# Kernel tuning notes

Measured on AMD Instinct MI355X. Metric: run time of the kernel, lower is better.

Reference implementation:

```python
import jax, jax.numpy as jnp
import numpy as np

B, T, D = 32, 1024, 192
HIDDEN = 4
CH = D * HIDDEN          # conv hidden channels = in_channel * hidden_size
K1, K2 = 5, 3
PAD = 3                  # (K1 - 1) // 2 + 1 for odd kernel_size=5 (ReplicationPad1d)
NUM_LEVELS = 3
N_NODES = 2 ** NUM_LEVELS - 1  # 7 Interaction blocks in the SCINet tree
OUT_LEN = 512


def setup_inputs() -> dict:
    key = jax.random.key(0)
    ks = jax.random.split(key, 6)
    s1 = 1.0 / np.sqrt(D * K1)   # torch Conv1d default init bound (fan_in = Cin*k)
    s2 = 1.0 / np.sqrt(CH * K2)
    sp = 1.0 / np.sqrt(T)
    x = jax.random.normal(ks[0], (B, T, D), dtype=jnp.float32)
    # Stacked params for all 7 tree nodes x 4 branches (phi, psi, eta, rho)
    W1 = jax.random.uniform(ks[1], (N_NODES, 4, CH, D, K1), jnp.float32, -s1, s1)
    b1 = jax.random.uniform(ks[2], (N_NODES, 4, CH), jnp.float32, -s1, s1)
    W2 = jax.random.uniform(ks[3], (N_NODES, 4, D, CH, K2), jnp.float32, -s2, s2)
    b2 = jax.random.uniform(ks[4], (N_NODES, 4, D), jnp.float32, -s2, s2)
    # projection1 = Conv1d(input_len, output_len, k=1, bias=False) over time-as-channels
    Wproj = jax.random.uniform(ks[5], (OUT_LEN, T), jnp.float32, -sp, sp)
    return {"x": x, "W1": W1, "b1": b1, "W2": W2, "b2": b2, "Wproj": Wproj}


def _conv1d(x, w, b):
    # x: (B, Cin, L), w: (Cout, Cin, K)
    y = jax.lax.conv_general_dilated(x, w, (1,), 'VALID',
                                     dimension_numbers=('NCH', 'OIH', 'NCH'))
    return y + b[None, :, None]


def _branch(x, w1, b1, w2, b2):
    # ReplicationPad1d(3,3) -> Conv(k=5) -> LeakyReLU -> (Dropout p=0) -> Conv(k=3) -> Tanh
    xp = jnp.pad(x, ((0, 0), (0, 0), (PAD, PAD)), mode='edge')
    h = jax.nn.leaky_relu(_conv1d(xp, w1, b1), 0.01)
    return jnp.tanh(_conv1d(h, w2, b2))  # length back to L


def _interact(x, w1, b1, w2, b2):
    # x: (B, T, D) -> even/odd (B, D, T/2)
    xe = jnp.transpose(x[:, ::2, :], (0, 2, 1))
    xo = jnp.transpose(x[:, 1::2, :], (0, 2, 1))
    d = xo * jnp.exp(_branch(xe, w1[0], b1[0], w2[0], b2[0]))  # phi
    c = xe * jnp.exp(_branch(xo, w1[1], b1[1], w2[1], b2[1]))  # psi
    even_up = c + _branch(d, w1[2], b1[2], w2[2], b2[2])        # eta
    odd_up = d - _branch(c, w1[3], b1[3], w2[3], b2[3])         # rho
    return jnp.transpose(even_up, (0, 2, 1)), jnp.transpose(odd_up, (0, 2, 1))


def _zip_up(even, odd):
    # interleave even/odd along time (equal lengths since T % 2**levels == 0)
    b, t, c = even.shape
    return jnp.stack([even, odd], axis=2).reshape(b, 2 * t, c)


def _tree(x, level, idx, W1, b1, W2, b2):
    i = idx[0]
    idx[0] += 1
    e, o = _interact(x, W1[i], b1[i], W2[i], b2[i])
    if level == 0:
        return _zip_up(e, o)
    return _zip_up(_tree(e, level - 1, idx, W1, b1, W2, b2),
                   _tree(o, level - 1, idx, W1, b1, W2, b2))


def reference(x, W1, b1, W2, b2, Wproj):
    out = _tree(x, NUM_LEVELS - 1, [0], W1, b1, W2, b2) + x  # residual
    # projection1: Conv1d over time-as-channels, kernel 1, no bias
    return jnp.einsum('btd,ot->bod', out, Wproj)
```

## Files before the change

kernel.cpp:

```cpp
#include <hip/hip_runtime.h>
#include <hip/hip_bf16.h>

typedef unsigned short u16;
typedef unsigned int u32;
typedef __bf16 bf16x8 __attribute__((ext_vector_type(8)));
typedef float f32x4 __attribute__((ext_vector_type(4)));

#define NB 32
#define NT 1024
#define ND 192
#define NCH 768
#define NOUT 512

__device__ __forceinline__ float bf2f(u16 x) { return __uint_as_float(((u32)x) << 16); }
__device__ __forceinline__ u16 f2bf(float f) {
    u32 u = __float_as_uint(f);
    return (u16)((u + 0x7fffu + ((u >> 16) & 1u)) >> 16);
}
__device__ __forceinline__ float tanh_fast(float x) {
    float e = __expf(2.f * x);
    return 1.f - 2.f / (e + 1.f);
}
__device__ __forceinline__ int xcd_swz(int bx, int nwg) {
    int q = nwg >> 3, r = nwg & 7;
    int xcd = bx & 7, idx = bx >> 3;
    return (xcd < r ? xcd * (q + 1) : r * (q + 1) + (xcd - r) * q) + idx;
}

__constant__ int NODE_IDX[3][4] = {{0, 0, 0, 0}, {1, 4, 0, 0}, {2, 5, 3, 6}};

__global__ void cvt8(const float* __restrict__ in, u16* __restrict__ out, int n8) {
    int i = blockIdx.x * 256 + threadIdx.x;
    if (i >= n8) return;
    const float4* p = (const float4*)in + 2 * (size_t)i;
    float4 a = p[0], c = p[1];
    uint4 o;
    o.x = f2bf(a.x) | ((u32)f2bf(a.y) << 16);
    o.y = f2bf(a.z) | ((u32)f2bf(a.w) << 16);
    o.z = f2bf(c.x) | ((u32)f2bf(c.y) << 16);
    o.w = f2bf(c.z) | ((u32)f2bf(c.w) << 16);
    ((uint4*)out)[i] = o;
}

__global__ __launch_bounds__(256) void w1fk(const float* __restrict__ W1, u16* __restrict__ W1f) {
    __shared__ u16 ls[32][968];
    const int nb = blockIdx.x / 24;
    const int cot = blockIdx.x % 24;
    const float* src = W1 + ((size_t)nb * NCH + cot * 32) * (ND * 5);
    for (int idx = threadIdx.x; idx < 7680; idx += 256) {
        int e4 = idx * 4;
        int rowc = e4 / 960, col = e4 % 960;
        float4 v = *(const float4*)(src + (size_t)rowc * 960 + col);
        ls[rowc][col + 0] = f2bf(v.x);
        ls[rowc][col + 1] = f2bf(v.y);
        ls[rowc][col + 2] = f2bf(v.z);
        ls[rowc][col + 3] = f2bf(v.w);
    }
    __syncthreads();
    const int lane = threadIdx.x & 63, sub = threadIdx.x >> 6;
    const int g = lane >> 4, r = lane & 15;
    for (int it = 0; it < 15; ++it) {
        int fid = it * 4 + sub;
        int kkb = fid >> 1, cobl = fid & 1;
        u16 tmp[8];
#pragma unroll
        for (int e = 0; e < 8; ++e) {
            int kk = kkb * 32 + 8 * g + e;
            int ci = kk % 192, k = kk / 192;
            tmp[e] = ls[cobl * 16 + r][ci * 5 + k];
        }
        uint4 o;
        o.x = tmp[0] | ((u32)tmp[1] << 16);
        o.y = tmp[2] | ((u32)tmp[3] << 16);
        o.z = tmp[4] | ((u32)tmp[5] << 16);
        o.w = tmp[6] | ((u32)tmp[7] << 16);
        size_t off = (((size_t)nb * 30 + kkb) * 48 + cot * 2 + cobl) * 512 + lane * 8;
        *(uint4*)(W1f + off) = o;
    }
}

__global__ __launch_bounds__(256) void w2fk(const float* __restrict__ W2, u16* __restrict__ W2f) {
    __shared__ u16 ls[16][1160];
    const int ch = blockIdx.x & 1;
    const int t = blockIdx.x >> 1;
    const int nb = t / 12, cot = t % 12;
    const float* src = W2 + ((size_t)nb * ND + cot * 16) * (NCH * 3) + ch * 1152;
    for (int idx = threadIdx.x; idx < 4608; idx += 256) {
        int e4 = idx * 4;
        int rowc = e4 / 1152, col = e4 % 1152;
        float4 v = *(const float4*)(src + (size_t)rowc * (NCH * 3) + col);
        ls[rowc][col + 0] = f2bf(v.x);
        ls[rowc][col + 1] = f2bf(v.y);
        ls[rowc][col + 2] = f2bf(v.z);
        ls[rowc][col + 3] = f2bf(v.w);
    }
    __syncthreads();
    const int lane = threadIdx.x & 63, sub = threadIdx.x >> 6;
    const int g = lane >> 4, r = lane & 15;
    for (int it = 0; it < 9; ++it) {
        int fid = it * 4 + sub;
        int k = fid / 12, cib = fid % 12;
        int kkb = k * 24 + ch * 12 + cib;
        u16 tmp[8];
#pragma unroll
        for (int e = 0; e < 8; ++e) {
            int cl = cib * 32 + 8 * g + e;
            tmp[e] = ls[r][cl * 3 + k];
        }
        uint4 o;
        o.x = tmp[0] | ((u32)tmp[1] << 16);
        o.y = tmp[2] | ((u32)tmp[3] << 16);
        o.z = tmp[4] | ((u32)tmp[5] << 16);
        o.w = tmp[6] | ((u32)tmp[7] << 16);
        size_t off = (((size_t)nb * 72 + kkb) * 12 + cot) * 512 + lane * 8;
        *(uint4*)(W2f + off) = o;
    }
}

__global__ __launch_bounds__(256) void conv1m(
    const u16* __restrict__ bufb, const u16* __restrict__ dbufb, const u16* __restrict__ cbufb,
    const u16* __restrict__ W1f, const float* __restrict__ b1,
    u16* __restrict__ h, int lvl, int stage) {
    const int L = 512 >> lvl, nodes = 1 << lvl, Lout = L + 2;
    const int tid = threadIdx.x;
    const int mT1 = (NB * Lout + 127) / 128;
    const int wg = xcd_swz(blockIdx.x, gridDim.x);
    const int z = wg / (6 * mT1);
    const int rem = wg - z * 6 * mT1;
    const int mt = rem / 6;
    const int cot = rem % 6;
    const int g_node = z & (nodes - 1);
    const int br = z >> lvl;
    const int nb4 = NODE_IDX[lvl][g_node] * 4 + (stage ? 2 + br : br);

    const int r0 = mt * 128;
    const int b0 = r0 / Lout;
    const int t00 = r0 - b0 * Lout;
    const int s = Lout - t00;
    const int rowsValid0 = NB * Lout - r0;
    const int rowsValid = rowsValid0 < 128 ? rowsValid0 : 128;

    __shared__ u16 xs[136 * 192];

    const int lane = tid & 63, w = tid >> 6;
    const int wrow = w >> 1, wcol = w & 1;
    const int lr = lane & 15, lg = lane >> 4;
    const u16* wf = W1f + ((size_t)nb4 * 30 * 48 + cot * 8 + wcol * 4) * 512 + lane * 8;

    bf16x8 Bb[3][4], Ab[2][4];
    auto loadB = [&](bf16x8(&dst)[4], int step) {
#pragma unroll
        for (int n = 0; n < 4; ++n)
            dst[n] = *(const bf16x8*)(wf + ((size_t)step * 48 + n) * 512);
    };
    loadB(Bb[0], 0);
    loadB(Bb[1], 1);

    const u16* dcb = br ? cbufb : dbufb;
    const int slot = g_node + (br << lvl);
    for (int ch = tid; ch < 136 * 24; ch += 256) {
        int j = ch / 24, c8 = ch % 24;
        int bb, u;
        if (j <= s + 3) { bb = b0; u = t00 - 3 + j; }
        else            { bb = b0 + 1; u = j - s - 7; }
        u = u < 0 ? 0 : (u > L - 1 ? L - 1 : u);
        if (bb > NB - 1) bb = NB - 1;
        const u16* p;
        if (stage == 0)
            p = bufb + ((size_t)bb * NT + slot + (size_t)u * (2 * nodes)) * ND + c8 * 8;
        else
            p = dcb + (((size_t)g_node * NB + bb) * L + u) * (size_t)ND + c8 * 8;
        *(uint4*)(xs + j * 192 + ((c8 * 8) ^ ((j & 7) << 3))) = *(const uint4*)p;
    }
    __syncthreads();

    int rowb[4];
#pragma unroll
    for (int m = 0; m < 4; ++m) {
        int i = wrow * 64 + m * 16 + lr;
        rowb[m] = i + (i >= s ? 4 : 0);
    }

    f32x4 acc[4][4];
    f32x4 zz = {0.f, 0.f, 0.f, 0.f};
#pragma unroll
    for (int m = 0; m < 4; ++m)
#pragma unroll
        for (int n = 0; n < 4; ++n) acc[m][n] = zz;

    auto loadA = [&](bf16x8(&dst)[4], int step) {
        const int k = step / 6, cib = step % 6;
#pragma unroll
        for (int m = 0; m < 4; ++m) {
            int row = rowb[m] + k;
            dst[m] = *(const bf16x8*)(xs + row * 192 + ((cib * 32 + lg * 8) ^ ((row & 7) << 3)));
        }
    };
    loadA(Ab[0], 0);
#pragma unroll
    for (int st = 0; st < 30; ++st) {
        if (st + 2 < 30) loadB(Bb[(st + 2) % 3], st + 2);
        if (st + 1 < 30) loadA(Ab[(st + 1) & 1], st + 1);
#pragma unroll
        for (int m = 0; m < 4; ++m)
#pragma unroll
            for (int n = 0; n < 4; ++n)
                acc[m][n] = __builtin_amdgcn_mfma_f32_16x16x32_bf16(
                    Ab[st & 1][m], Bb[st % 3][n], acc[m][n], 0, 0, 0);
    }

    float bias[4];
    const float* bb1 = b1 + (size_t)nb4 * NCH + cot * 128 + wcol * 64 + lr;
#pragma unroll
    for (int n = 0; n < 4; ++n) bias[n] = bb1[n * 16];
    u16* hz = h + (size_t)z * NB * Lout * NCH;
#pragma unroll
    for (int m = 0; m < 4; ++m) {
#pragma unroll
        for (int rr = 0; rr < 4; ++rr) {
            int i = wrow * 64 + m * 16 + lg * 4 + rr;
            if (i < rowsValid) {
                int cross = (i >= s) ? 1 : 0;
                int bb = b0 + cross;
                int tt = cross ? i - s : t00 + i;
                u16* dst = hz + ((size_t)bb * Lout + tt) * NCH + cot * 128 + wcol * 64 + lr;
#pragma unroll
                for (int n = 0; n < 4; ++n) {
                    float v = acc[m][n][rr] + bias[n];
                    v = v > 0.f ? v : 0.01f * v;
                    dst[n * 16] = f2bf(v);
                }
            }
        }
    }
}

__global__ __launch_bounds__(512) void conv2m(
    u16* __restrict__ bufb, u16* __restrict__ dbufb, u16* __restrict__ cbufb,
    const u16* __restrict__ W2f, const float* __restrict__ b2,
    const u16* __restrict__ h, int lvl, int stage) {
    const int L = 512 >> lvl, nodes = 1 << lvl, Lout = L + 2;
    const int tid = threadIdx.x;
    const int nM = (NB * L) >> 7;
    const int wg = xcd_swz(blockIdx.x, gridDim.x);
    const int z = wg / nM;
    const int mt = wg - z * nM;
    const int g_node = z & (nodes - 1);
    const int br = z >> lvl;
    const int nb4 = NODE_IDX[lvl][g_node] * 4 + (stage ? 2 + br : br);
    const int r0 = mt * 128;
    const int b = r0 >> (9 - lvl);
    const int t0 = r0 & (L - 1);

    __shared__ u16 xs[130 * 192];
    const u16* hz = h + ((size_t)z * NB + b) * Lout * NCH;

    const int lane = tid & 63, w = tid >> 6;
    const int wrow = w >> 2, wcol = w & 3;
    const int lr = lane & 15, lg = lane >> 4;
    const u16* wf = W2f + ((size_t)nb4 * 72 * 12 + wcol * 3) * 512 + lane * 8;

    auto kkb_of = [](int st) {
        int cc = st / 18, sp = st % 18;
        return (sp / 6) * 24 + cc * 6 + (sp % 6);
    };
    bf16x8 Bb[4][3], Ab[2][4];
    auto loadB = [&](bf16x8(&dst)[3], int st) {
        const size_t kb = (size_t)kkb_of(st) * 12 * 512;
#pragma unroll
        for (int n = 0; n < 3; ++n)
            dst[n] = *(const bf16x8*)(wf + kb + (size_t)n * 512);
    };
    auto loadA = [&](bf16x8(&dst)[4], int sp) {
        const int k = sp / 6, cj = sp % 6;
#pragma unroll
        for (int m = 0; m < 4; ++m) {
            int row = wrow * 64 + m * 16 + lr + k;
            dst[m] = *(const bf16x8*)(xs + row * 192 + ((cj * 32 + lg * 8) ^ ((row & 7) << 3)));
        }
    };
    loadB(Bb[0], 0);
    loadB(Bb[1], 1);
    loadB(Bb[2], 2);

    f32x4 acc[4][3];
    f32x4 zz = {0.f, 0.f, 0.f, 0.f};
#pragma unroll
    for (int m = 0; m < 4; ++m)
#pragma unroll
        for (int n = 0; n < 3; ++n) acc[m][n] = zz;

#pragma unroll
    for (int cc = 0; cc < 4; ++cc) {
        __syncthreads();
        for (int ch = tid; ch < 130 * 24; ch += 512) {
            int j = ch / 24, c8 = ch % 24;
            *(uint4*)(xs + j * 192 + ((c8 * 8) ^ ((j & 7) << 3))) =
                *(const uint4*)(hz + (size_t)(t0 + j) * NCH + cc * 192 + c8 * 8);
        }
        __syncthreads();
        loadA(Ab[0], 0);
#pragma unroll
        for (int sp = 0; sp < 18; ++sp) {
            int st = cc * 18 + sp;
            if (st + 3 < 72) loadB(Bb[(st + 3) & 3], st + 3);
            if (sp + 1 < 18) loadA(Ab[(sp + 1) & 1], sp + 1);
#pragma unroll
            for (int m = 0; m < 4; ++m)
#pragma unroll
                for (int n = 0; n < 3; ++n)
                    acc[m][n] = __builtin_amdgcn_mfma_f32_16x16x32_bf16(
                        Ab[sp & 1][m], Bb[st & 3][n], acc[m][n], 0, 0, 0);
        }
    }

    float bias[3];
    const float* bb2 = b2 + (size_t)nb4 * ND + wcol * 48 + lr;
#pragma unroll
    for (int n = 0; n < 3; ++n) bias[n] = bb2[n * 16];

    const int tstr = 2 * nodes;
    if (stage == 0) {
        const int mo = g_node + (br == 0 ? nodes : 0);
        const u16* mult = bufb + ((size_t)b * NT + mo) * ND;
        u16* dst = (br == 0 ? dbufb : cbufb) + ((size_t)g_node * NB + b) * (size_t)L * ND;
#pragma unroll
        for (int m = 0; m < 4; ++m) {
#pragma unroll
            for (int rr = 0; rr < 4; ++rr) {
                int i = wrow * 64 + m * 16 + lg * 4 + rr;
                int t = t0 + i;
#pragma unroll
                for (int n = 0; n < 3; ++n) {
                    int co = wcol * 48 + n * 16 + lr;
                    float v = tanh_fast(acc[m][n][rr] + bias[n]);
                    float mlt = bf2f(mult[(size_t)t * tstr * ND + co]);
                    dst[(size_t)t * ND + co] = f2bf(mlt * __expf(v));
                }
            }
        }
    } else {
        const u16* other = (br == 0 ? cbufb : dbufb) + ((size_t)g_node * NB + b) * (size_t)L * ND;
        const int to = g_node + (br ? nodes : 0);
        u16* dst = bufb + ((size_t)b * NT + to) * ND;
#pragma unroll
        for (int m = 0; m < 4; ++m) {
#pragma unroll
            for (int rr = 0; rr < 4; ++rr) {
                int i = wrow * 64 + m * 16 + lg * 4 + rr;
                int t = t0 + i;
#pragma unroll
                for (int n = 0; n < 3; ++n) {
                    int co = wcol * 48 + n * 16 + lr;
                    float v = tanh_fast(acc[m][n][rr] + bias[n]);
                    float o = bf2f(other[(size_t)t * ND + co]);
                    dst[(size_t)t * tstr * ND + co] = f2bf(br == 0 ? o + v : o - v);
                }
            }
        }
    }
}

__global__ __launch_bounds__(256) void mkin2T(const u16* __restrict__ bufb,
                                              const float* __restrict__ x,
                                              u16* __restrict__ in2T) {
    __shared__ u16 ls[64][72];
    const int b = blockIdx.z, t0 = blockIdx.y * 64, d0 = blockIdx.x * 64;
    const int tid = threadIdx.x;
#pragma unroll
    for (int it = 0; it < 2; ++it) {
        int idx = tid + it * 256;
        int c8 = idx >> 6, row = idx & 63;
        size_t base = ((size_t)b * NT + t0 + row) * ND + d0 + c8 * 8;
        uint4 vb = *(const uint4*)(bufb + base);
        float4 x1 = *(const float4*)(x + base);
        float4 x2 = *(const float4*)(x + base + 4);
        const u16* vs = (const u16*)&vb;
        ls[c8 * 8 + 0][row] = f2bf(bf2f(vs[0]) + x1.x);
        ls[c8 * 8 + 1][row] = f2bf(bf2f(vs[1]) + x1.y);
        ls[c8 * 8 + 2][row] = f2bf(bf2f(vs[2]) + x1.z);
        ls[c8 * 8 + 3][row] = f2bf(bf2f(vs[3]) + x1.w);
        ls[c8 * 8 + 4][row] = f2bf(bf2f(vs[4]) + x2.x);
        ls[c8 * 8 + 5][row] = f2bf(bf2f(vs[5]) + x2.y);
        ls[c8 * 8 + 6][row] = f2bf(bf2f(vs[6]) + x2.z);
        ls[c8 * 8 + 7][row] = f2bf(bf2f(vs[7]) + x2.w);
    }
    __syncthreads();
#pragma unroll
    for (int it = 0; it < 2; ++it) {
        int idx = tid + it * 256;
        int dl = idx >> 3, t8 = idx & 7;
        uint4 v = *(uint4*)&ls[dl][t8 * 8];
        *(uint4*)(in2T + ((size_t)b * ND + d0 + dl) * NT + t0 + t8 * 8) = v;
    }
}

__global__ __launch_bounds__(256) void projm(const u16* __restrict__ in2T,
                                             const u16* __restrict__ Wpb,
                                             float* __restrict__ out) {
    const int b = blockIdx.y, ot = blockIdx.x;
    const int tid = threadIdx.x, lane = tid & 63, w = tid >> 6;
    const int lr = lane & 15, lg = lane >> 4;
    const u16* ap = Wpb + ((size_t)(ot * 32 + lr)) * NT + lg * 8;
    const u16* bp = in2T + ((size_t)b * ND + w * 48 + lr) * NT + lg * 8;

    f32x4 acc[2][3];
    f32x4 zz = {0.f, 0.f, 0.f, 0.f};
#pragma unroll
    for (int m = 0; m < 2; ++m)
#pragma unroll
        for (int n = 0; n < 3; ++n) acc[m][n] = zz;

    auto loadA = [&](bf16x8(&dst)[2], int kkb) {
#pragma unroll
        for (int m = 0; m < 2; ++m)
            dst[m] = *(const bf16x8*)(ap + (size_t)m * 16 * NT + kkb * 32);
    };
    auto loadB = [&](bf16x8(&dst)[3], int kkb) {
#pragma unroll
        for (int n = 0; n < 3; ++n)
            dst[n] = *(const bf16x8*)(bp + (size_t)n * 16 * NT + kkb * 32);
    };
    auto domfma = [&](bf16x8(&A)[2], bf16x8(&B)[3]) {
#pragma unroll
        for (int m = 0; m < 2; ++m)
#pragma unroll
            for (int n = 0; n < 3; ++n)
                acc[m][n] = __builtin_amdgcn_mfma_f32_16x16x32_bf16(A[m], B[n], acc[m][n], 0, 0, 0);
    };

    bf16x8 Ab[2][2], Bb[3][3];
    loadA(Ab[0], 0);
    loadB(Bb[0], 0);
    loadB(Bb[1], 1);
#pragma unroll
    for (int sp = 0; sp < 32; ++sp) {
        if (sp + 2 < 32) loadB(Bb[(sp + 2) % 3], sp + 2);
        if (sp + 1 < 32) loadA(Ab[(sp + 1) & 1], sp + 1);
        domfma(Ab[sp & 1], Bb[sp % 3]);
    }

#pragma unroll
    for (int m = 0; m < 2; ++m)
#pragma unroll
        for (int rr = 0; rr < 4; ++rr) {
            int o = ot * 32 + m * 16 + lg * 4 + rr;
#pragma unroll
            for (int n = 0; n < 3; ++n) {
                int d = w * 48 + n * 16 + lr;
                out[((size_t)b * NOUT + o) * ND + d] = acc[m][n][rr];
            }
        }
}

extern "C" void kernel_launch(void* const* d_in, const int* in_sizes, int n_in,
                              void* d_out, int out_size, void* d_ws, size_t ws_size,
                              hipStream_t stream) {
    const float* x = (const float*)d_in[0];
    const float* W1 = (const float*)d_in[1];
    const float* b1 = (const float*)d_in[2];
    const float* W2 = (const float*)d_in[3];
    const float* b2 = (const float*)d_in[4];
    const float* Wp = (const float*)d_in[5];
    float* out = (float*)d_out;

    char* wsb = (char*)d_ws;
    size_t off = 0;
    auto carve = [&](size_t bytes) {
        void* p = wsb + off;
        off += (bytes + 255) & ~(size_t)255;
        return p;
    };
    const size_t w1f_e = (size_t)28 * 30 * 48 * 512;
    const size_t w2f_e = (size_t)28 * 72 * 12 * 512;
    const size_t wpb_e = (size_t)NOUT * NT;
    const size_t buf_e = (size_t)NB * NT * ND;
    const size_t dc_e = (size_t)NB * 512 * ND;
    const size_t h_e = (size_t)1040 * NB * NCH;
    const size_t i2_e = (size_t)NB * ND * NT;

    u16* W1f = (u16*)carve(sizeof(u16) * w1f_e);
    u16* W2f = (u16*)carve(sizeof(u16) * w2f_e);
    u16* Wpb = (u16*)carve(sizeof(u16) * wpb_e);
    u16* bufb = (u16*)carve(sizeof(u16) * buf_e);
    u16* dbufb = (u16*)carve(sizeof(u16) * dc_e);
    u16* cbufb = (u16*)carve(sizeof(u16) * dc_e);
    u16* h = (u16*)carve(sizeof(u16) * h_e);
    u16* in2T = (u16*)carve(sizeof(u16) * i2_e);
    if (off > ws_size) return;

    cvt8<<<(int)(buf_e / 8 / 256), 256, 0, stream>>>(x, bufb, (int)(buf_e / 8));
    cvt8<<<(int)(wpb_e / 8 / 256), 256, 0, stream>>>(Wp, Wpb, (int)(wpb_e / 8));
    w1fk<<<28 * 24, 256, 0, stream>>>(W1, W1f);
    w2fk<<<28 * 12 * 2, 256, 0, stream>>>(W2, W2f);

    for (int lvl = 0; lvl < 3; ++lvl) {
        int L = 512 >> lvl, nodes = 1 << lvl, Lout = L + 2;
        int mT1 = (NB * Lout + 127) / 128;
        int nM = NB * L / 128;
        dim3 g1(6 * mT1 * 2 * nodes);
        dim3 g2(nM * 2 * nodes);
        conv1m<<<g1, 256, 0, stream>>>(bufb, dbufb, cbufb, W1f, b1, h, lvl, 0);
        conv2m<<<g2, 512, 0, stream>>>(bufb, dbufb, cbufb, W2f, b2, h, lvl, 0);
        conv1m<<<g1, 256, 0, stream>>>(bufb, dbufb, cbufb, W1f, b1, h, lvl, 1);
        conv2m<<<g2, 512, 0, stream>>>(bufb, dbufb, cbufb, W2f, b2, h, lvl, 1);
    }
    mkin2T<<<dim3(3, 16, NB), 256, 0, stream>>>(bufb, x, in2T);
    projm<<<dim3(16, NB), 256, 0, stream>>>(in2T, Wpb, out);
}
```

Baseline: 774.2 us.

## Stage conv1 weight tiles into a triple-buffered LDS ring via global_load_lds

In the first-conv MFMA kernel, each wave used to load its B (weight) fragments straight from global memory into registers. Now the whole workgroup copies each weight K-step into one of three LDS slots with direct global-to-LDS loads, and waves read their fragments from LDS. This removes duplicate global weight reads between waves that share a column tile. In exchange it adds a vmcnt wait and a workgroup barrier every step, and 24 KB more LDS, which may lower occupancy.

```diff
diff --git a/kernel.cpp b/kernel.cpp
--- a/kernel.cpp
+++ b/kernel.cpp
@@ -26,6 +26,13 @@
     int xcd = bx & 7, idx = bx >> 3;
     return (xcd < r ? xcd * (q + 1) : r * (q + 1) + (xcd - r) * q) + idx;
 }
+__device__ __forceinline__ void gl_lds16(const u16* g, u16* l) {
+    __builtin_amdgcn_global_load_lds(
+        (const __attribute__((address_space(1))) void*)g,
+        (__attribute__((address_space(3))) void*)l, 16, 0, 0);
+}
+#define VMCNT2 asm volatile("s_waitcnt vmcnt(2)" ::: "memory")
+#define VMCNT0 asm volatile("s_waitcnt vmcnt(0)" ::: "memory")
 
 __constant__ int NODE_IDX[3][4] = {{0, 0, 0, 0}, {1, 4, 0, 0}, {2, 5, 3, 6}};
 
@@ -141,23 +148,24 @@
     const int rowsValid = rowsValid0 < 128 ? rowsValid0 : 128;
 
     __shared__ u16 xs[136 * 192];
+    __shared__ u16 bs[3 * 4096];
 
     const int lane = tid & 63, w = tid >> 6;
     const int wrow = w >> 1, wcol = w & 1;
     const int lr = lane & 15, lg = lane >> 4;
-    const u16* wf = W1f + ((size_t)nb4 * 30 * 48 + cot * 8 + wcol * 4) * 512 + lane * 8;
-
-    bf16x8 Bb[3][4], Ab[2][4];
-    auto loadB = [&](bf16x8(&dst)[4], int step) {
-#pragma unroll
-        for (int n = 0; n < 4; ++n)
-            dst[n] = *(const bf16x8*)(wf + ((size_t)step * 48 + n) * 512);
-    };
-    loadB(Bb[0], 0);
-    loadB(Bb[1], 1);
+
+    const u16* wsrc = W1f + ((size_t)nb4 * 30 * 48 + cot * 8) * 512;
+    auto stageB = [&](int kkb, int slot) {
+        const u16* gp = wsrc + (size_t)kkb * (48 * 512) + tid * 8;
+        u16* lp = bs + slot * 4096 + tid * 8;
+        gl_lds16(gp, lp);
+        gl_lds16(gp + 2048, lp + 2048);
+    };
+    stageB(0, 0);
+    stageB(1, 1);
 
     const u16* dcb = br ? cbufb : dbufb;
-    const int slot = g_node + (br << lvl);
+    const int slot_in = g_node + (br << lvl);
     for (int ch = tid; ch < 136 * 24; ch += 256) {
         int j = ch / 24, c8 = ch % 24;
         int bb, u;
@@ -167,7 +175,7 @@
         if (bb > NB - 1) bb = NB - 1;
         const u16* p;
         if (stage == 0)
-            p = bufb + ((size_t)bb * NT + slot + (size_t)u * (2 * nodes)) * ND + c8 * 8;
+            p = bufb + ((size_t)bb * NT + slot_in + (size_t)u * (2 * nodes)) * ND + c8 * 8;
         else
             p = dcb + (((size_t)g_node * NB + bb) * L + u) * (size_t)ND + c8 * 8;
         *(uint4*)(xs + j * 192 + ((c8 * 8) ^ ((j & 7) << 3))) = *(const uint4*)p;
@@ -180,6 +188,7 @@
         int i = wrow * 64 + m * 16 + lr;
         rowb[m] = i + (i >= s ? 4 : 0);
     }
+    const int lg8 = lg * 8;
 
     f32x4 acc[4][4];
     f32x4 zz = {0.f, 0.f, 0.f, 0.f};
@@ -193,20 +202,34 @@
 #pragma unroll
         for (int m = 0; m < 4; ++m) {
             int row = rowb[m] + k;
-            dst[m] = *(const bf16x8*)(xs + row * 192 + ((cib * 32 + lg * 8) ^ ((row & 7) << 3)));
-        }
-    };
-    loadA(Ab[0], 0);
-#pragma unroll
-    for (int st = 0; st < 30; ++st) {
-        if (st + 2 < 30) loadB(Bb[(st + 2) % 3], st + 2);
-        if (st + 1 < 30) loadA(Ab[(st + 1) & 1], st + 1);
-#pragma unroll
-        for (int m = 0; m < 4; ++m)
-#pragma unroll
-            for (int n = 0; n < 4; ++n)
+            dst[m] = *(const bf16x8*)(xs + row * 192 + ((cib * 32 + lg8) ^ ((row & 7) << 3)));
+        }
+    };
+
+    bf16x8 Ap[2][4];
+    loadA(Ap[0], 0);
+
+#pragma unroll
+    for (int j = 0; j < 30; ++j) {
+        if (j + 2 < 30) stageB(j + 2, (j + 2) % 3);
+        bf16x8 Bf[4];
+#pragma unroll
+        for (int n = 0; n < 4; ++n)
+            Bf[n] = *(const bf16x8*)(bs + (j % 3) * 4096 + (wcol * 4 + n) * 512 + lane * 8);
+        if (j + 1 < 30) loadA(Ap[(j + 1) & 1], j + 1);
+#pragma unroll
+        for (int n = 0; n < 4; ++n)
+#pragma unroll
+            for (int m = 0; m < 4; ++m)
                 acc[m][n] = __builtin_amdgcn_mfma_f32_16x16x32_bf16(
-                    Ab[st & 1][m], Bb[st % 3][n], acc[m][n], 0, 0, 0);
+                    Ap[j & 1][m], Bf[n], acc[m][n], 0, 0, 0);
+        if (j < 28) {
+            VMCNT2;
+            __builtin_amdgcn_s_barrier();
+        } else if (j == 28) {
+            VMCNT0;
+            __builtin_amdgcn_s_barrier();
+        }
     }
 
     float bias[4];
```

Result: slower. 840.5 us (+8.6%).

## Stream conv1 A/B tiles into double-buffered LDS via direct global-to-LDS loads

Applied to the files above, without the earlier changes.

conv1m no longer stages the whole 136x192 input tile in LDS up front, and no longer prefetches weights from global into registers. Both the activation slices (32 input channels per step) and the weight fragments are now copied with global_load_lds into two ping-pong LDS buffers. The loop runs channel-block outer and kernel tap inner, with a barrier after each step. The aim is to cut LDS footprint so more blocks fit per CU, drop register pressure from the weight prefetch, and overlap global loads with MFMA work. The cost is 29 block barriers per tile. The XCD-aware block swizzle is also removed in favour of a 3D grid, which may hurt L2 locality of weights.

```diff
diff --git a/kernel.cpp b/kernel.cpp
--- a/kernel.cpp
+++ b/kernel.cpp
@@ -25,6 +25,11 @@
     int q = nwg >> 3, r = nwg & 7;
     int xcd = bx & 7, idx = bx >> 3;
     return (xcd < r ? xcd * (q + 1) : r * (q + 1) + (xcd - r) * q) + idx;
+}
+__device__ __forceinline__ void gl_lds16(const u16* g, u16* l) {
+    __builtin_amdgcn_global_load_lds(
+        (const __attribute__((address_space(1))) void*)g,
+        (__attribute__((address_space(3))) void*)l, 16, 0, 0);
 }
 
 __constant__ int NODE_IDX[3][4] = {{0, 0, 0, 0}, {1, 4, 0, 0}, {2, 5, 3, 6}};
@@ -123,12 +128,9 @@
     u16* __restrict__ h, int lvl, int stage) {
     const int L = 512 >> lvl, nodes = 1 << lvl, Lout = L + 2;
     const int tid = threadIdx.x;
-    const int mT1 = (NB * Lout + 127) / 128;
-    const int wg = xcd_swz(blockIdx.x, gridDim.x);
-    const int z = wg / (6 * mT1);
-    const int rem = wg - z * 6 * mT1;
-    const int mt = rem / 6;
-    const int cot = rem % 6;
+    const int cot = blockIdx.x % 6;
+    const int mt = blockIdx.x / 6;
+    const int z = blockIdx.z;
     const int g_node = z & (nodes - 1);
     const int br = z >> lvl;
     const int nb4 = NODE_IDX[lvl][g_node] * 4 + (stage ? 2 + br : br);
@@ -140,38 +142,48 @@
     const int rowsValid0 = NB * Lout - r0;
     const int rowsValid = rowsValid0 < 128 ? rowsValid0 : 128;
 
-    __shared__ u16 xs[136 * 192];
+    __shared__ u16 a_lds[2][136 * 32];
+    __shared__ u16 b_lds[2][4096];
 
     const int lane = tid & 63, w = tid >> 6;
     const int wrow = w >> 1, wcol = w & 1;
     const int lr = lane & 15, lg = lane >> 4;
-    const u16* wf = W1f + ((size_t)nb4 * 30 * 48 + cot * 8 + wcol * 4) * 512 + lane * 8;
-
-    bf16x8 Bb[3][4], Ab[2][4];
-    auto loadB = [&](bf16x8(&dst)[4], int step) {
-#pragma unroll
-        for (int n = 0; n < 4; ++n)
-            dst[n] = *(const bf16x8*)(wf + ((size_t)step * 48 + n) * 512);
-    };
-    loadB(Bb[0], 0);
-    loadB(Bb[1], 1);
+
+    const u16* wsrc = W1f + ((size_t)nb4 * 30 * 48 + cot * 8) * 512;
+    auto stageB = [&](int st, int bufi) {
+        const int cib = st / 5, k = st % 5;
+        const int kkb = k * 6 + cib;
+        const u16* gp = wsrc + (size_t)kkb * (48 * 512) + tid * 8;
+        gl_lds16(gp, &b_lds[bufi][tid * 8]);
+        gl_lds16(gp + 2048, &b_lds[bufi][tid * 8 + 2048]);
+    };
 
     const u16* dcb = br ? cbufb : dbufb;
     const int slot = g_node + (br << lvl);
-    for (int ch = tid; ch < 136 * 24; ch += 256) {
-        int j = ch / 24, c8 = ch % 24;
-        int bb, u;
-        if (j <= s + 3) { bb = b0; u = t00 - 3 + j; }
-        else            { bb = b0 + 1; u = j - s - 7; }
-        u = u < 0 ? 0 : (u > L - 1 ? L - 1 : u);
-        if (bb > NB - 1) bb = NB - 1;
-        const u16* p;
-        if (stage == 0)
-            p = bufb + ((size_t)bb * NT + slot + (size_t)u * (2 * nodes)) * ND + c8 * 8;
-        else
-            p = dcb + (((size_t)g_node * NB + bb) * L + u) * (size_t)ND + c8 * 8;
-        *(uint4*)(xs + j * 192 + ((c8 * 8) ^ ((j & 7) << 3))) = *(const uint4*)p;
-    }
+    auto stageA = [&](int cib, int bufi) {
+#pragma unroll
+        for (int inst = 0; inst < 3; ++inst) {
+            if (inst == 2 && tid >= 32) continue;
+            int unit = inst * 256 + tid;
+            int j = unit >> 2, cp = unit & 3;
+            int gc = cp ^ ((j >> 1) & 3);
+            int bb, u;
+            if (j <= s + 3) { bb = b0; u = t00 - 3 + j; }
+            else            { bb = b0 + 1; u = j - s - 7; }
+            u = u < 0 ? 0 : (u > L - 1 ? L - 1 : u);
+            if (bb > NB - 1) bb = NB - 1;
+            const u16* p;
+            if (stage == 0)
+                p = bufb + ((size_t)bb * NT + slot + (size_t)u * (2 * nodes)) * ND;
+            else
+                p = dcb + (((size_t)g_node * NB + bb) * L + u) * (size_t)ND;
+            gl_lds16(p + cib * 32 + gc * 8, &a_lds[bufi][unit * 8]);
+        }
+    };
+
+    stageA(0, 0);
+    stageB(0, 0);
+    stageA(1, 1);
     __syncthreads();
 
     int rowb[4];
@@ -188,25 +200,27 @@
 #pragma unroll
         for (int n = 0; n < 4; ++n) acc[m][n] = zz;
 
-    auto loadA = [&](bf16x8(&dst)[4], int step) {
-        const int k = step / 6, cib = step % 6;
+#pragma unroll
+    for (int st = 0; st < 30; ++st) {
+        const int cib = st / 5, k = st % 5;
+        if (st + 1 < 30) stageB(st + 1, (st + 1) & 1);
+        if (k == 0 && cib >= 1 && cib < 5) stageA(cib + 1, (cib + 1) & 1);
+        bf16x8 Ar[4], Br[4];
 #pragma unroll
         for (int m = 0; m < 4; ++m) {
-            int row = rowb[m] + k;
-            dst[m] = *(const bf16x8*)(xs + row * 192 + ((cib * 32 + lg * 8) ^ ((row & 7) << 3)));
-        }
-    };
-    loadA(Ab[0], 0);
-#pragma unroll
-    for (int st = 0; st < 30; ++st) {
-        if (st + 2 < 30) loadB(Bb[(st + 2) % 3], st + 2);
-        if (st + 1 < 30) loadA(Ab[(st + 1) & 1], st + 1);
+            int r = rowb[m] + k;
+            Ar[m] = *(const bf16x8*)(&a_lds[cib & 1][r * 32 + ((lg ^ ((r >> 1) & 3)) * 8)]);
+        }
+#pragma unroll
+        for (int n = 0; n < 4; ++n)
+            Br[n] = *(const bf16x8*)(&b_lds[st & 1][(wcol * 4 + n) * 512 + lane * 8]);
 #pragma unroll
         for (int m = 0; m < 4; ++m)
 #pragma unroll
             for (int n = 0; n < 4; ++n)
                 acc[m][n] = __builtin_amdgcn_mfma_f32_16x16x32_bf16(
-                    Ab[st & 1][m], Bb[st % 3][n], acc[m][n], 0, 0, 0);
+                    Ar[m], Br[n], acc[m][n], 0, 0, 0);
+        if (st < 29) __syncthreads();
     }
 
     float bias[4];
@@ -498,7 +512,7 @@
         int L = 512 >> lvl, nodes = 1 << lvl, Lout = L + 2;
         int mT1 = (NB * Lout + 127) / 128;
         int nM = NB * L / 128;
-        dim3 g1(6 * mT1 * 2 * nodes);
+        dim3 g1(6 * mT1, 1, 2 * nodes);
         dim3 g2(nM * 2 * nodes);
         conv1m<<<g1, 256, 0, stream>>>(bufb, dbufb, cbufb, W1f, b1, h, lvl, 0);
         conv2m<<<g2, 512, 0, stream>>>(bufb, dbufb, cbufb, W2f, b2, h, lvl, 0);
```

New measurement: 845.1 us. 1.09x slower.
